# Kernel tuning notes

Measured on AMD Instinct MI355X. Metric: run time of the kernel, lower is better.

## Reference

```python
import jax, jax.numpy as jnp
import numpy as np

EPS = 1e-8
LN_EPS = 1e-5
TOPK = 8

B, N, D = 8, 2048, 512


def setup_inputs() -> dict:
    key = jax.random.key(0)
    ks = jax.random.split(key, 4)
    feats = jax.random.normal(ks[0], (B, N, D), dtype=jnp.float32)
    mask = jnp.ones((B, N), dtype=bool)
    # per-layer GCN weights (no bias) and LayerNorm params, plus output LN
    W1 = jax.random.normal(ks[1], (D, D), dtype=jnp.float32) / np.sqrt(D)
    W2 = jax.random.normal(ks[2], (D, D), dtype=jnp.float32) / np.sqrt(D)
    ln1_g = jnp.ones((D,), jnp.float32); ln1_b = jnp.zeros((D,), jnp.float32)
    ln2_g = jnp.ones((D,), jnp.float32); ln2_b = jnp.zeros((D,), jnp.float32)
    out_g = jnp.ones((D,), jnp.float32); out_b = jnp.zeros((D,), jnp.float32)
    return {"feats": feats, "mask": mask, "W1": W1, "ln1_g": ln1_g, "ln1_b": ln1_b,
            "W2": W2, "ln2_g": ln2_g, "ln2_b": ln2_b, "out_g": out_g, "out_b": out_b}


def _layer_norm(x, g, b):
    mu = jnp.mean(x, axis=-1, keepdims=True)
    var = jnp.mean(jnp.square(x - mu), axis=-1, keepdims=True)
    return (x - mu) * jax.lax.rsqrt(var + LN_EPS) * g + b


def build_similarity_graph(feats, mask):
    b, n, _ = feats.shape
    mask_f = mask.astype(feats.dtype)                       # [B,N]
    valid_pair = mask[:, None, :] & mask[:, :, None]        # [B,N,N]
    vp_f = valid_pair.astype(feats.dtype)
    # cosine similarity mapped to [0,1]
    fn = feats / jnp.clip(jnp.linalg.norm(feats, axis=-1, keepdims=True), EPS)
    sim = (jnp.einsum('bnd,bmd->bnm', fn, fn) + 1.0) * 0.5
    sim = sim * vp_f
    eye = jnp.eye(n, dtype=bool)
    sim_wo_self = jnp.where(eye[None], 0.0, sim)
    # top-k neighbors per node (invalid pairs pushed to -1)
    k = min(TOPK, n - 1)
    candidate = jnp.where(valid_pair, sim_wo_self, -1.0)
    values, indices = jax.lax.top_k(candidate, k)           # [B,N,k]
    bi = jnp.arange(b)[:, None, None]
    ri = jnp.arange(n)[None, :, None]
    knn_mask = jnp.zeros((b, n, n), dtype=bool).at[bi, ri, indices].set(values > 0)
    adj = sim_wo_self * knn_mask.astype(feats.dtype)
    # symmetrize, add valid self-loops, re-mask
    adj = 0.5 * (adj + jnp.swapaxes(adj, 1, 2))
    adj = adj + jnp.eye(n, dtype=feats.dtype)[None] * (mask_f[:, :, None] * mask_f[:, None, :])
    adj = adj * vp_f
    # symmetric degree normalization
    deg_inv_sqrt = jnp.clip(adj.sum(-1), EPS) ** -0.5       # [B,N]
    adj_norm = adj * deg_inv_sqrt[:, :, None] * deg_inv_sqrt[:, None, :]
    return adj_norm * vp_f


def _gcn_layer(x, adj_norm, W, g, b, mask_f):
    out = jnp.einsum('bnm,bmd->bnd', adj_norm, x @ W) + x   # residual (Identity proj)
    out = jax.nn.relu(_layer_norm(out, g, b))
    return out * mask_f[..., None]


def reference(feats, mask, W1, ln1_g, ln1_b, W2, ln2_g, ln2_b, out_g, out_b):
    mask_f = mask.astype(feats.dtype)
    x = feats * mask_f[..., None]                           # input_proj = Identity, then mask
    adj_norm = build_similarity_graph(feats, mask)
    x = _gcn_layer(x, adj_norm, W1, ln1_g, ln1_b, mask_f)
    x = _gcn_layer(x, adj_norm, W2, ln2_g, ln2_b, mask_f)
    x = _layer_norm(x, out_g, out_b)
    return x * mask_f[..., None]
```

## Files before the change

kernel.cpp:

```cpp
#include <hip/hip_runtime.h>
#include <cstdint>


constexpr int Bb   = 8;
constexpr int Nn   = 2048;
constexpr int Dd   = 512;
constexpr int BN   = Bb * Nn;
constexpr int KTOP = 8;
constexpr int CAP  = 56;
constexpr int NSLICE = 8;

typedef __attribute__((ext_vector_type(8))) __bf16 bf16x8;
typedef __attribute__((ext_vector_type(4))) __bf16 bf16x4;
typedef __attribute__((ext_vector_type(4))) float  f32x4;

__device__ __forceinline__ void gload16(const void* g, void* l) {
  __builtin_amdgcn_global_load_lds((const __attribute__((address_space(1))) unsigned int*)g,
                                   (__attribute__((address_space(3))) unsigned int*)l,
                                   16, 0, 0);
}
__device__ __forceinline__ void barrier_raw() {
  asm volatile("" ::: "memory");
  __builtin_amdgcn_s_barrier();
  asm volatile("" ::: "memory");
}
__device__ __forceinline__ unsigned umax_(unsigned a, unsigned b) { return a > b ? a : b; }
__device__ __forceinline__ unsigned umin_(unsigned a, unsigned b) { return a > b ? b : a; }

__global__ __launch_bounds__(256) void prep_kernel(const float* __restrict__ feats,
                                                   float* __restrict__ rinv,
                                                   float* __restrict__ normv,
                                                   __bf16* __restrict__ Hk,
                                                   int* __restrict__ ecnt,
                                                   const float* __restrict__ W1,
                                                   const float* __restrict__ W2,
                                                   __bf16* __restrict__ Wk1,
                                                   __bf16* __restrict__ Wk2) {
  __shared__ float tile[32][65];
  __shared__ float rsh[32];
  const int t = threadIdx.x;

  if (blockIdx.x >= 512) {
    const int idx = blockIdx.x - 512;
    const float* W = (idx >> 8) ? W2 : W1;
    __bf16* Wk     = (idx >> 8) ? Wk2 : Wk1;
    const int rem = idx & 255;
    const int bx = (rem & 15) * 32, by = (rem >> 4) * 32;
    __shared__ float tt[32][33];
    const int lx = t & 31, ly = t >> 5;
#pragma unroll
    for (int r = 0; r < 32; r += 8)
      tt[ly + r][lx] = W[(size_t)(by + ly + r) * Dd + bx + lx];
    __syncthreads();
    if (t < 128) {
      const int k8l = t >> 5, nl = t & 31;
      bf16x8 v;
#pragma unroll
      for (int e = 0; e < 8; ++e) v[e] = (__bf16)tt[k8l * 8 + e][nl];
      *(bf16x8*)(Wk + ((size_t)((by >> 3) + k8l) * Dd + bx + nl) * 8) = v;
    }
    return;
  }

  const int r0 = blockIdx.x * 32;
  const int bz = r0 >> 11;
  const int n0 = r0 & 2047;
  const int wv = t >> 6, lane = t & 63;

  if (t < 32) ecnt[r0 + t] = 0;

  for (int i = 0; i < 8; ++i) {
    const int row = wv * 8 + i;
    const float* p = feats + (size_t)(r0 + row) * Dd + lane * 8;
    float4 a = *(const float4*)p;
    float4 b = *(const float4*)(p + 4);
    float s = a.x*a.x + a.y*a.y + a.z*a.z + a.w*a.w
            + b.x*b.x + b.y*b.y + b.z*b.z + b.w*b.w;
#pragma unroll
    for (int o = 32; o; o >>= 1) s += __shfl_down(s, o);
    if (lane == 0) {
      const float nr = fmaxf(sqrtf(s), 1e-8f);
      rsh[row] = 1.0f / nr;
      rinv[r0 + row]  = 1.0f / nr;
      normv[r0 + row] = nr;
    }
  }

  for (int kt = 0; kt < 8; ++kt) {
    __syncthreads();
    {
      const int row = t >> 3, ch = t & 7;
      const float* p = feats + (size_t)(r0 + row) * Dd + kt * 64 + ch * 8;
      float4 v0 = *(const float4*)p;
      float4 v1 = *(const float4*)(p + 4);
      tile[row][ch * 8 + 0] = v0.x; tile[row][ch * 8 + 1] = v0.y;
      tile[row][ch * 8 + 2] = v0.z; tile[row][ch * 8 + 3] = v0.w;
      tile[row][ch * 8 + 4] = v1.x; tile[row][ch * 8 + 5] = v1.y;
      tile[row][ch * 8 + 6] = v1.z; tile[row][ch * 8 + 7] = v1.w;
    }
    __syncthreads();
    {
      const int k8l = t >> 5, row = t & 31;
      const float s = rsh[row];
      bf16x8 hv;
#pragma unroll
      for (int e = 0; e < 8; ++e) hv[e] = (__bf16)(tile[row][k8l * 8 + e] * s);
      *(bf16x8*)(Hk + ((size_t)(bz * 64) + (size_t)(kt * 8 + k8l)) * (Nn * 8)
                    + (n0 + row) * 8) = hv;
    }
  }
}

__device__ __forceinline__ void ins8t(float (&tv)[8], int (&ti)[8], float v, int idx) {
#pragma unroll
  for (int q = 0; q < 8; ++q) {
    bool sw = (v > tv[q]) || (v == tv[q] && idx < ti[q]);
    float a = sw ? tv[q] : v;
    int   c = sw ? ti[q] : idx;
    tv[q] = sw ? v   : tv[q];
    ti[q] = sw ? idx : ti[q];
    v = a; idx = c;
  }
}

__device__ __forceinline__ void gemm_core(const __bf16* __restrict__ Ab, int Astr, int mloc,
                                          const __bf16* __restrict__ Wk, int m0, int n0,
                                          __bf16* __restrict__ Yb, int tid, char* smem) {
  const int lane   = tid & 63;
  const int lane15 = tid & 15;
  const int kgrp   = (tid >> 4) & 3;
  const int wv     = tid >> 6;
  const int wrow0  = wv * 32;

  auto stage = [&](int t, int buf) {
    const int k80 = t << 2;
#pragma unroll
    for (int i = 0; i < 4; ++i) {
      const int c = (wv << 2) + i;
      const bool isB = c >= 8;
      const int cc = isB ? c - 8 : c;
      const int kg = cc >> 1, rb = cc & 1;
      const __bf16* g = isB
          ? Wk + ((size_t)(k80 + kg) * Dd + n0 + rb * 64 + lane) * 8
          : Ab + ((size_t)(k80 + kg) * Astr + mloc + rb * 64 + lane) * 8;
      gload16(g, smem + buf * 16384 + (isB ? 8192 : 0) + kg * 2048 + (rb * 64 + lane) * 16);
    }
  };

  f32x4 acc[2][8];
  const f32x4 z = {0.f, 0.f, 0.f, 0.f};
#pragma unroll
  for (int i = 0; i < 2; ++i)
#pragma unroll
    for (int j = 0; j < 8; ++j) acc[i][j] = z;

  stage(0, 0);
  for (int t = 0; t < 16; ++t) {
    const int cur = t & 1;
    if (t + 1 < 16) {
      stage(t + 1, cur ^ 1);
      asm volatile("s_waitcnt vmcnt(4)" ::: "memory");
    } else {
      asm volatile("s_waitcnt vmcnt(0)" ::: "memory");
    }
    barrier_raw();

    const char* sb = smem + cur * 16384;
    const int a0o = kgrp * 2048 + (wrow0 + lane15) * 16;
    bf16x8 a0 = *(const bf16x8*)(sb + a0o);
    bf16x8 a1 = *(const bf16x8*)(sb + a0o + 256);
#pragma unroll
    for (int cs = 0; cs < 8; ++cs) {
      bf16x8 b = *(const bf16x8*)(sb + 8192 + kgrp * 2048 + (cs * 16 + lane15) * 16);
      acc[0][cs] = __builtin_amdgcn_mfma_f32_16x16x32_bf16(b, a0, acc[0][cs], 0, 0, 0);
      acc[1][cs] = __builtin_amdgcn_mfma_f32_16x16x32_bf16(b, a1, acc[1][cs], 0, 0, 0);
    }
    barrier_raw();
  }
#pragma unroll
  for (int rs = 0; rs < 2; ++rs) {
    const int row = m0 + wv * 32 + rs * 16 + lane15;
#pragma unroll
    for (int cs = 0; cs < 8; ++cs) {
      bf16x4 o;
#pragma unroll
      for (int e = 0; e < 4; ++e) o[e] = (__bf16)acc[rs][cs][e];
      *(bf16x4*)(Yb + (size_t)row * Dd + n0 + cs * 16 + kgrp * 4) = o;
    }
  }
}

__global__ __launch_bounds__(256, 4) void sim_gemm_kernel(const __bf16* __restrict__ Hk,
                                                          const __bf16* __restrict__ Wk1,
                                                          __bf16* __restrict__ Yb,
                                                          float* __restrict__ pv,
                                                          int* __restrict__ pi) {
  __shared__ __align__(16) char smem[32768];
  const int tid = threadIdx.x;

  if (blockIdx.x < 512) {
    const int gb = blockIdx.x;
    const int m0 = (gb >> 2) * 128, n0 = (gb & 3) * 128;
    const __bf16* Ab = Hk + (size_t)((m0 >> 11) * 64) * (Nn * 8);
    gemm_core(Ab, Nn, m0 & 2047, Wk1, m0, n0, Yb, tid, smem);
    return;
  }

  const int f     = blockIdx.x - 512;
  const int bz    = f & 7;
  const int rr    = f >> 3;
  const int r0    = (rr & 15) * 128;
  const int slice = rr >> 4;

  const int lane   = tid & 63;
  const int lane15 = tid & 15;
  const int kgrp   = (tid >> 4) & 3;
  const int wv     = tid >> 6;
  const int wrow0  = wv * 32;
  const int bN     = bz * Nn;

  const __bf16* Hb = Hk + (size_t)(bz * 64) * (Nn * 8);

  unsigned t8k[2][8];
#pragma unroll
  for (int rs = 0; rs < 2; ++rs)
#pragma unroll
    for (int q = 0; q < 8; ++q) t8k[rs][q] = 0u;

  auto stage = [&](int t, int buf) {
    const int ct = t >> 4, k80 = (t & 15) << 2;
    const int c0 = slice * 256 + ct * 128;
#pragma unroll
    for (int i = 0; i < 4; ++i) {
      const int c = (wv << 2) + i;
      const bool isB = c >= 8;
      const int cc = isB ? c - 8 : c;
      const int kg = cc >> 1, rb = cc & 1;
      const int rbase = (isB ? c0 : r0) + rb * 64 + lane;
      gload16(Hb + ((size_t)(k80 + kg) * Nn + rbase) * 8,
              smem + buf * 16384 + (isB ? 8192 : 0) + kg * 2048 + (rb * 64 + lane) * 16);
    }
  };

  f32x4 acc[2][8];
  const f32x4 z = {0.f, 0.f, 0.f, 0.f};

  stage(0, 0);
  for (int t = 0; t < 32; ++t) {
    const int cur = t & 1;
    if ((t & 15) == 0) {
#pragma unroll
      for (int i = 0; i < 2; ++i)
#pragma unroll
        for (int j = 0; j < 8; ++j) acc[i][j] = z;
    }
    if (t + 1 < 32) {
      stage(t + 1, cur ^ 1);
      asm volatile("s_waitcnt vmcnt(4)" ::: "memory");
    } else {
      asm volatile("s_waitcnt vmcnt(0)" ::: "memory");
    }
    barrier_raw();

    const char* sb = smem + cur * 16384;
    const int a0o = kgrp * 2048 + (wrow0 + lane15) * 16;
    bf16x8 ah0 = *(const bf16x8*)(sb + a0o);
    bf16x8 ah1 = *(const bf16x8*)(sb + a0o + 256);
#pragma unroll
    for (int cs = 0; cs < 8; ++cs) {
      bf16x8 bh = *(const bf16x8*)(sb + 8192 + kgrp * 2048 + (cs * 16 + lane15) * 16);
      acc[0][cs] = __builtin_amdgcn_mfma_f32_16x16x32_bf16(bh, ah0, acc[0][cs], 0, 0, 0);
      acc[1][cs] = __builtin_amdgcn_mfma_f32_16x16x32_bf16(bh, ah1, acc[1][cs], 0, 0, 0);
    }
    barrier_raw();

    if ((t & 15) == 15) {
      const int ctile0 = slice * 256 + (t >> 4) * 128;
#pragma unroll
      for (int rs = 0; rs < 2; ++rs) {
        const int rowg = r0 + wrow0 + rs * 16 + lane15;
#pragma unroll
        for (int cs = 0; cs < 8; ++cs) {
          const int colb = ctile0 + cs * 16 + kgrp * 4;
#pragma unroll
          for (int e = 0; e < 4; ++e) {
            const int col = colb + e;
            unsigned key = (__float_as_uint(acc[rs][cs][e] + 2.0f) & 0xFFFFF800u)
                         | (unsigned)(0x7FF - col);
            key = (col == rowg) ? 0u : key;
#pragma unroll
            for (int q = 0; q < 8; ++q) {
              const unsigned hi = umax_(t8k[rs][q], key);
              key = umin_(t8k[rs][q], key);
              t8k[rs][q] = hi;
            }
          }
        }
      }
    }
  }

#pragma unroll
  for (int rs = 0; rs < 2; ++rs) {
#pragma unroll
    for (int m = 16; m <= 32; m <<= 1) {
      unsigned ok[8];
#pragma unroll
      for (int q = 0; q < 8; ++q) ok[q] = (unsigned)__shfl_xor((int)t8k[rs][q], m);
#pragma unroll
      for (int q = 0; q < 8; ++q) {
        unsigned key = ok[q];
#pragma unroll
        for (int p = 0; p < 8; ++p) {
          const unsigned hi = umax_(t8k[rs][p], key);
          key = umin_(t8k[rs][p], key);
          t8k[rs][p] = hi;
        }
      }
    }
  }

  if (lane < 16) {
#pragma unroll
    for (int rs = 0; rs < 2; ++rs) {
      const int prow = bN + r0 + wrow0 + rs * 16 + lane15;
#pragma unroll
      for (int q = 0; q < 8; ++q) {
        const unsigned key = t8k[rs][q];
        const int col = 0x7FF - (int)(key & 0x7FFu);
        const float raw = __uint_as_float(key & 0xFFFFF800u) - 2.0f;
        pv[((size_t)prow * NSLICE + slice) * 8 + q] = fmaxf((raw + 1.0f) * 0.5f, 0.0f);
        pi[((size_t)prow * NSLICE + slice) * 8 + q] = bN + col;
      }
    }
  }
}

__global__ __launch_bounds__(256, 4) void gemm2_kernel(const __bf16* __restrict__ Ak,
                                                       const __bf16* __restrict__ Wk,
                                                       __bf16* __restrict__ Yb) {
  __shared__ __align__(16) char smem[32768];
  const int gb = blockIdx.x;
  const int m0 = (gb >> 2) * 128, n0 = (gb & 3) * 128;
  gemm_core(Ak, BN, m0, Wk, m0, n0, Yb, threadIdx.x, smem);
}

__global__ __launch_bounds__(256) void refine_edges(const float* __restrict__ feats,
                                                    const float* __restrict__ rinv,
                                                    const float* __restrict__ pv,
                                                    const int* __restrict__ pi,
                                                    int* __restrict__ ecnt,
                                                    int* __restrict__ eidx,
                                                    float* __restrict__ ew) {
  const int f  = blockIdx.x;
  const int bz = f & 7;
  const int wv = threadIdx.x >> 6;
  const int lane = threadIdx.x & 63;
  const int bN = bz * Nn;
  const int row = bN + (f >> 3) * 4 + wv;

  const float scr = pv[(size_t)row * 64 + lane];
  const int   sid = pi[(size_t)row * 64 + lane];
  unsigned key = (__float_as_uint(scr) & 0xFFFFF800u) | (unsigned)(0x7FF - (sid - bN));

  const float* xi = feats + (size_t)row * Dd + lane * 8;
  const float4 xi0 = *(const float4*)xi;
  const float4 xi1 = *(const float4*)(xi + 4);
  const float  ri  = rinv[row];

  int ridx[12];
#pragma unroll
  for (int c = 0; c < 12; ++c) {
    unsigned m = key;
#pragma unroll
    for (int o = 32; o; o >>= 1) {
      const unsigned om = __shfl_xor(m, o);
      m = om > m ? om : m;
    }
    if (key == m) key = 0u;
    ridx[c] = bN + (0x7FF - (int)(m & 0x7FFu));
  }

  float rv[12];
#pragma unroll
  for (int c = 0; c < 12; c += 2) {
    const float* xa = feats + (size_t)ridx[c]     * Dd + lane * 8;
    const float* xb = feats + (size_t)ridx[c + 1] * Dd + lane * 8;
    const float4 a0 = *(const float4*)xa;
    const float4 a1 = *(const float4*)(xa + 4);
    const float4 b0 = *(const float4*)xb;
    const float4 b1 = *(const float4*)(xb + 4);
    float da = xi0.x*a0.x + xi0.y*a0.y + xi0.z*a0.z + xi0.w*a0.w
             + xi1.x*a1.x + xi1.y*a1.y + xi1.z*a1.z + xi1.w*a1.w;
    float db = xi0.x*b0.x + xi0.y*b0.y + xi0.z*b0.z + xi0.w*b0.w
             + xi1.x*b1.x + xi1.y*b1.y + xi1.z*b1.z + xi1.w*b1.w;
#pragma unroll
    for (int o = 32; o; o >>= 1) { da += __shfl_xor(da, o); db += __shfl_xor(db, o); }
    rv[c]     = (da * ri * rinv[ridx[c]]     + 1.0f) * 0.5f;
    rv[c + 1] = (db * ri * rinv[ridx[c + 1]] + 1.0f) * 0.5f;
  }

  float t8v[8]; int t8i[8];
#pragma unroll
  for (int q = 0; q < 8; ++q) { t8v[q] = -1.0f; t8i[q] = 0x7fffffff; }
#pragma unroll
  for (int c = 0; c < 12; ++c) ins8t(t8v, t8i, rv[c], ridx[c]);

  if (lane == 0) {
#pragma unroll
    for (int q = 0; q < KTOP; ++q) {
      if (t8v[q] > 0.0f) {
        const int j = t8i[q];
        const float w = 0.5f * t8v[q];
        int p = atomicAdd(&ecnt[row], 1);
        if (p < CAP) { eidx[row * CAP + p] = j; ew[row * CAP + p] = w; }
        int q2 = atomicAdd(&ecnt[j], 1);
        if (q2 < CAP) { eidx[j * CAP + q2] = row; ew[j * CAP + q2] = w; }
      }
    }
  }
}

__global__ __launch_bounds__(256) void deg_kernel(const int* __restrict__ ecnt,
                                                  const float* __restrict__ ew,
                                                  const float* __restrict__ normv,
                                                  float* __restrict__ dis,
                                                  float* __restrict__ dn) {
  const int r = blockIdx.x * 256 + threadIdx.x;
  if (r >= BN) return;
  const int cnt = min(ecnt[r], CAP);
  float d = 1.0f;
  for (int e = 0; e < cnt; ++e) d += ew[r * CAP + e];
  const float di = rsqrtf(fmaxf(d, 1e-8f));
  dis[r] = di;
  dn[r]  = di * normv[r];
}

template <bool FINAL>
__global__ __launch_bounds__(256) void agg_ln_kernel(const __bf16* __restrict__ yb,
                                                     const float* __restrict__ xres_f,
                                                     const __bf16* __restrict__ xres_k,
                                                     const int* __restrict__ ecnt,
                                                     const int* __restrict__ eidx,
                                                     const float* __restrict__ ew,
                                                     const float* __restrict__ dis,
                                                     const float* __restrict__ dwv,
                                                     const float* __restrict__ g1,
                                                     const float* __restrict__ b1v,
                                                     const float* __restrict__ g2,
                                                     const float* __restrict__ b2v,
                                                     float* __restrict__ outf,
                                                     __bf16* __restrict__ outk) {
  const int bz = blockIdx.x & 7;
  const int rr = blockIdx.x >> 3;
  const int wv = threadIdx.x >> 6;
  const int lane = threadIdx.x & 63;
  const int row = bz * Nn + rr * 4 + wv;
  const int d0 = lane * 8;

  const float di = dis[row];
  const float swt = di * dwv[row];

  bf16x8 yv = *(const bf16x8*)(yb + (size_t)row * Dd + d0);
  float a[8];
#pragma unroll
  for (int e2 = 0; e2 < 8; ++e2) a[e2] = swt * (float)yv[e2];

  const int cnt = min(ecnt[row], CAP);
  int e = 0;
  for (; e + 4 <= cnt; e += 4) {
    const int j0 = eidx[row * CAP + e];
    const int j1 = eidx[row * CAP + e + 1];
    const int j2 = eidx[row * CAP + e + 2];
    const int j3 = eidx[row * CAP + e + 3];
    const float c0 = ew[row * CAP + e]     * di * dwv[j0];
    const float c1 = ew[row * CAP + e + 1] * di * dwv[j1];
    const float c2 = ew[row * CAP + e + 2] * di * dwv[j2];
    const float c3 = ew[row * CAP + e + 3] * di * dwv[j3];
    bf16x8 v0 = *(const bf16x8*)(yb + (size_t)j0 * Dd + d0);
    bf16x8 v1 = *(const bf16x8*)(yb + (size_t)j1 * Dd + d0);
    bf16x8 v2 = *(const bf16x8*)(yb + (size_t)j2 * Dd + d0);
    bf16x8 v3 = *(const bf16x8*)(yb + (size_t)j3 * Dd + d0);
#pragma unroll
    for (int e2 = 0; e2 < 8; ++e2)
      a[e2] += c0 * (float)v0[e2] + c1 * (float)v1[e2]
             + c2 * (float)v2[e2] + c3 * (float)v3[e2];
  }
  for (; e < cnt; ++e) {
    const int j = eidx[row * CAP + e];
    const float c = ew[row * CAP + e] * di * dwv[j];
    bf16x8 v = *(const bf16x8*)(yb + (size_t)j * Dd + d0);
#pragma unroll
    for (int e2 = 0; e2 < 8; ++e2) a[e2] += c * (float)v[e2];
  }

  if (FINAL) {
    bf16x8 u = *(const bf16x8*)(xres_k + ((size_t)lane * BN + row) * 8);
#pragma unroll
    for (int e2 = 0; e2 < 8; ++e2) a[e2] += (float)u[e2];
  } else {
    const float* xp = xres_f + (size_t)row * Dd + d0;
    float4 x0 = *(const float4*)xp;
    float4 x1 = *(const float4*)(xp + 4);
    a[0] += x0.x; a[1] += x0.y; a[2] += x0.z; a[3] += x0.w;
    a[4] += x1.x; a[5] += x1.y; a[6] += x1.z; a[7] += x1.w;
  }

  float s = 0.f, qq = 0.f;
#pragma unroll
  for (int e2 = 0; e2 < 8; ++e2) { s += a[e2]; qq += a[e2] * a[e2]; }
#pragma unroll
  for (int o = 32; o; o >>= 1) { s += __shfl_xor(s, o); qq += __shfl_xor(qq, o); }
  const float mu = s * (1.0f / Dd);
  const float var = qq * (1.0f / Dd) - mu * mu;
  const float rs = rsqrtf(var + 1e-5f);

  const float* gp = g1 + d0;
  const float* bp = b1v + d0;
  float4 g0 = *(const float4*)gp,  g1v = *(const float4*)(gp + 4);
  float4 bb0 = *(const float4*)bp, bb1 = *(const float4*)(bp + 4);
  float tv[8];
  tv[0] = fmaxf((a[0] - mu) * rs * g0.x + bb0.x, 0.0f);
  tv[1] = fmaxf((a[1] - mu) * rs * g0.y + bb0.y, 0.0f);
  tv[2] = fmaxf((a[2] - mu) * rs * g0.z + bb0.z, 0.0f);
  tv[3] = fmaxf((a[3] - mu) * rs * g0.w + bb0.w, 0.0f);
  tv[4] = fmaxf((a[4] - mu) * rs * g1v.x + bb1.x, 0.0f);
  tv[5] = fmaxf((a[5] - mu) * rs * g1v.y + bb1.y, 0.0f);
  tv[6] = fmaxf((a[6] - mu) * rs * g1v.z + bb1.z, 0.0f);
  tv[7] = fmaxf((a[7] - mu) * rs * g1v.w + bb1.w, 0.0f);

  if (FINAL) {
    float s2 = 0.f, q2 = 0.f;
#pragma unroll
    for (int e2 = 0; e2 < 8; ++e2) { s2 += tv[e2]; q2 += tv[e2] * tv[e2]; }
#pragma unroll
    for (int o = 32; o; o >>= 1) { s2 += __shfl_xor(s2, o); q2 += __shfl_xor(q2, o); }
    const float mu2 = s2 * (1.0f / Dd);
    const float var2 = q2 * (1.0f / Dd) - mu2 * mu2;
    const float rs2 = rsqrtf(var2 + 1e-5f);
    const float* g2p = g2 + d0;
    const float* b2p = b2v + d0;
    float4 G0 = *(const float4*)g2p,  G1 = *(const float4*)(g2p + 4);
    float4 B0 = *(const float4*)b2p,  B1 = *(const float4*)(b2p + 4);
    float4 o0, o1;
    o0.x = (tv[0] - mu2) * rs2 * G0.x + B0.x;
    o0.y = (tv[1] - mu2) * rs2 * G0.y + B0.y;
    o0.z = (tv[2] - mu2) * rs2 * G0.z + B0.z;
    o0.w = (tv[3] - mu2) * rs2 * G0.w + B0.w;
    o1.x = (tv[4] - mu2) * rs2 * G1.x + B1.x;
    o1.y = (tv[5] - mu2) * rs2 * G1.y + B1.y;
    o1.z = (tv[6] - mu2) * rs2 * G1.z + B1.z;
    o1.w = (tv[7] - mu2) * rs2 * G1.w + B1.w;
    float* op = outf + (size_t)row * Dd + d0;
    *(float4*)op = o0;
    *(float4*)(op + 4) = o1;
  } else {
    bf16x8 ov;
#pragma unroll
    for (int e2 = 0; e2 < 8; ++e2) ov[e2] = (__bf16)tv[e2];
    *(bf16x8*)(outk + ((size_t)lane * BN + row) * 8) = ov;
  }
}

extern "C" void kernel_launch(void* const* d_in, const int* in_sizes, int n_in,
                              void* d_out, int out_size, void* d_ws, size_t ws_size,
                              hipStream_t stream) {
  const float* feats = (const float*)d_in[0];
  const float* W1    = (const float*)d_in[2];
  const float* ln1_g = (const float*)d_in[3];
  const float* ln1_b = (const float*)d_in[4];
  const float* W2    = (const float*)d_in[5];
  const float* ln2_g = (const float*)d_in[6];
  const float* ln2_b = (const float*)d_in[7];
  const float* out_g = (const float*)d_in[8];
  const float* out_b = (const float*)d_in[9];
  float* out = (float*)d_out;

  char* w = (char*)d_ws;
  float* rinv  = (float*)w; w += (size_t)BN * 4;
  float* normv = (float*)w; w += (size_t)BN * 4;
  int*   ecnt  = (int*)w;   w += (size_t)BN * 4;
  int*   eidx  = (int*)w;   w += (size_t)BN * CAP * 4;
  float* ew    = (float*)w; w += (size_t)BN * CAP * 4;
  float* dis   = (float*)w; w += (size_t)BN * 4;
  float* dn    = (float*)w; w += (size_t)BN * 4;
  __bf16* Wk1  = (__bf16*)w; w += (size_t)Dd * Dd * 2;
  __bf16* Wk2  = (__bf16*)w; w += (size_t)Dd * Dd * 2;
  __bf16* Hk   = (__bf16*)w; w += (size_t)BN * Dd * 2;
  __bf16* Yb   = (__bf16*)w; w += (size_t)BN * Dd * 2;
  __bf16* h1k  = (__bf16*)w; w += (size_t)BN * Dd * 2;
  float* pv  = (float*)h1k;
  int*   pi  = (int*)((char*)h1k + (size_t)BN * NSLICE * 8 * 4);

  prep_kernel<<<1024, 256, 0, stream>>>(feats, rinv, normv, Hk, ecnt,
                                        W1, W2, Wk1, Wk2);

  sim_gemm_kernel<<<1536, 256, 0, stream>>>(Hk, Wk1, Yb, pv, pi);

  refine_edges<<<BN / 4, 256, 0, stream>>>(feats, rinv, pv, pi, ecnt, eidx, ew);
  deg_kernel<<<BN / 256, 256, 0, stream>>>(ecnt, ew, normv, dis, dn);

  agg_ln_kernel<false><<<BN / 4, 256, 0, stream>>>(Yb, feats, nullptr, ecnt, eidx, ew,
                                                   dis, dn, ln1_g, ln1_b,
                                                   nullptr, nullptr, nullptr, h1k);
  gemm2_kernel<<<512, 256, 0, stream>>>(h1k, Wk2, Yb);
  agg_ln_kernel<true><<<BN / 4, 256, 0, stream>>>(Yb, nullptr, h1k, ecnt, eidx, ew,
                                                  dis, dis, ln2_g, ln2_b,
                                                  out_g, out_b, out, nullptr);
}
```

Measured before the change: 278.8 us.

## Fuse degree computation into refine_edges via per-batch last-block counter

```diff
diff --git a/kernel.cpp b/kernel.cpp
--- a/kernel.cpp
+++ b/kernel.cpp
@@ -32,6 +32,7 @@
                                                    float* __restrict__ normv,
                                                    __bf16* __restrict__ Hk,
                                                    int* __restrict__ ecnt,
+                                                   int* __restrict__ batch_done,
                                                    const float* __restrict__ W1,
                                                    const float* __restrict__ W2,
                                                    __bf16* __restrict__ Wk1,
@@ -68,6 +69,7 @@
   const int wv = t >> 6, lane = t & 63;
 
   if (t < 32) ecnt[r0 + t] = 0;
+  if (blockIdx.x == 0 && t < 8) batch_done[t] = 0;
 
   for (int i = 0; i < 8; ++i) {
     const int row = wv * 8 + i;
@@ -200,9 +202,12 @@
 
   if (blockIdx.x < 512) {
     const int gb = blockIdx.x;
-    const int m0 = (gb >> 2) * 128, n0 = (gb & 3) * 128;
-    const __bf16* Ab = Hk + (size_t)((m0 >> 11) * 64) * (Nn * 8);
-    gemm_core(Ab, Nn, m0 & 2047, Wk1, m0, n0, Yb, tid, smem);
+    const int bz = gb & 7;
+    const int idx = gb >> 3;
+    const int m0 = bz * Nn + (idx >> 2) * 128;
+    const int n0 = (idx & 3) * 128;
+    const __bf16* Ab = Hk + (size_t)(bz * 64) * (Nn * 8);
+    gemm_core(Ab, Nn, (idx >> 2) * 128, Wk1, m0, n0, Yb, tid, smem);
     return;
   }
 
@@ -341,7 +346,10 @@
                                                        __bf16* __restrict__ Yb) {
   __shared__ __align__(16) char smem[32768];
   const int gb = blockIdx.x;
-  const int m0 = (gb >> 2) * 128, n0 = (gb & 3) * 128;
+  const int bz = gb & 7;
+  const int idx = gb >> 3;
+  const int m0 = bz * Nn + (idx >> 2) * 128;
+  const int n0 = (idx & 3) * 128;
   gemm_core(Ak, BN, m0, Wk, m0, n0, Yb, threadIdx.x, smem);
 }
 
@@ -351,13 +359,20 @@
                                                     const int* __restrict__ pi,
                                                     int* __restrict__ ecnt,
                                                     int* __restrict__ eidx,
-                                                    float* __restrict__ ew) {
+                                                    float* __restrict__ ew,
+                                                    const float* __restrict__ normv,
+                                                    float* __restrict__ dis,
+                                                    float* __restrict__ dn,
+                                                    int* __restrict__ batch_done) {
+  __shared__ int lastf;
   const int f  = blockIdx.x;
   const int bz = f & 7;
   const int wv = threadIdx.x >> 6;
   const int lane = threadIdx.x & 63;
   const int bN = bz * Nn;
   const int row = bN + (f >> 3) * 4 + wv;
+
+  if (threadIdx.x == 0) lastf = 0;
 
   const float scr = pv[(size_t)row * 64 + lane];
   const int   sid = pi[(size_t)row * 64 + lane];
@@ -418,22 +433,25 @@
         if (q2 < CAP) { eidx[j * CAP + q2] = row; ew[j * CAP + q2] = w; }
       }
     }
-  }
-}
-
-__global__ __launch_bounds__(256) void deg_kernel(const int* __restrict__ ecnt,
-                                                  const float* __restrict__ ew,
-                                                  const float* __restrict__ normv,
-                                                  float* __restrict__ dis,
-                                                  float* __restrict__ dn) {
-  const int r = blockIdx.x * 256 + threadIdx.x;
-  if (r >= BN) return;
-  const int cnt = min(ecnt[r], CAP);
-  float d = 1.0f;
-  for (int e = 0; e < cnt; ++e) d += ew[r * CAP + e];
-  const float di = rsqrtf(fmaxf(d, 1e-8f));
-  dis[r] = di;
-  dn[r]  = di * normv[r];
+    __threadfence();
+  }
+  __syncthreads();
+  if (threadIdx.x == 0) {
+    if (atomicAdd(&batch_done[bz], 1) == 511) lastf = 1;
+  }
+  __syncthreads();
+  if (lastf) {
+    __threadfence();
+    for (int i = threadIdx.x; i < Nn; i += 256) {
+      const int r = bN + i;
+      const int cnt2 = min(ecnt[r], CAP);
+      float d = 1.0f;
+      for (int e2 = 0; e2 < cnt2; ++e2) d += ew[r * CAP + e2];
+      const float di2 = rsqrtf(fmaxf(d, 1e-8f));
+      dis[r] = di2;
+      dn[r]  = di2 * normv[r];
+    }
+  }
 }
 
 template <bool FINAL>
@@ -584,6 +602,7 @@
   float* ew    = (float*)w; w += (size_t)BN * CAP * 4;
   float* dis   = (float*)w; w += (size_t)BN * 4;
   float* dn    = (float*)w; w += (size_t)BN * 4;
+  int*   bdone = (int*)w;   w += 64;
   __bf16* Wk1  = (__bf16*)w; w += (size_t)Dd * Dd * 2;
   __bf16* Wk2  = (__bf16*)w; w += (size_t)Dd * Dd * 2;
   __bf16* Hk   = (__bf16*)w; w += (size_t)BN * Dd * 2;
@@ -592,13 +611,13 @@
   float* pv  = (float*)h1k;
   int*   pi  = (int*)((char*)h1k + (size_t)BN * NSLICE * 8 * 4);
 
-  prep_kernel<<<1024, 256, 0, stream>>>(feats, rinv, normv, Hk, ecnt,
+  prep_kernel<<<1024, 256, 0, stream>>>(feats, rinv, normv, Hk, ecnt, bdone,
                                         W1, W2, Wk1, Wk2);
 
   sim_gemm_kernel<<<1536, 256, 0, stream>>>(Hk, Wk1, Yb, pv, pi);
 
-  refine_edges<<<BN / 4, 256, 0, stream>>>(feats, rinv, pv, pi, ecnt, eidx, ew);
-  deg_kernel<<<BN / 256, 256, 0, stream>>>(ecnt, ew, normv, dis, dn);
+  refine_edges<<<BN / 4, 256, 0, stream>>>(feats, rinv, pv, pi, ecnt, eidx, ew,
+                                           normv, dis, dn, bdone);
 
   agg_ln_kernel<false><<<BN / 4, 256, 0, stream>>>(Yb, feats, nullptr, ecnt, eidx, ew,
                                                    dis, dn, ln1_g, ln1_b,
```

New measurement: 717.6 us. +157.4%, slower.
